# Kernel optimization log

Measured on AMD Instinct MI355X. Metric: run time of the kernel, lower is better.

Reference implementation:

```python
import jax, jax.numpy as jnp
import numpy as np

D_MODEL = 1024
NUM_HEADS = 16
HEAD_DIM = D_MODEL // NUM_HEADS
B, S = 2, 2048


def setup_inputs() -> dict:
    key = jax.random.key(0)
    ks = jax.random.split(key, 10)
    sc = 1.0 / np.sqrt(D_MODEL)
    return {
        "x": jax.random.normal(ks[0], (B, S, D_MODEL), jnp.float32),
        "y": jax.random.normal(ks[1], (B, S, D_MODEL), jnp.float32),
        "Wkv": jax.random.normal(ks[2], (D_MODEL, 2 * D_MODEL), jnp.float32) * sc,
        "bkv": jax.random.normal(ks[3], (2 * D_MODEL,), jnp.float32) * 0.01,
        "Wq": jax.random.normal(ks[4], (D_MODEL, D_MODEL), jnp.float32) * sc,
        "bq": jax.random.normal(ks[5], (D_MODEL,), jnp.float32) * 0.01,
        "Wo": jax.random.normal(ks[6], (D_MODEL, D_MODEL), jnp.float32) * sc,
        "bo": jax.random.normal(ks[7], (D_MODEL,), jnp.float32) * 0.01,
    }


def reference(x, y, Wkv, bkv, Wq, bq, Wo, bo):
    b, s, d = x.shape
    # projections: kv from x (keys/values come from encoder side), q from y
    kv = x @ Wkv + bkv                      # [B, S, 2*d_model]
    q = y @ Wq + bq                         # [B, S, d_model]
    kv = kv.reshape(b, s, NUM_HEADS, 2 * HEAD_DIM).transpose(0, 2, 1, 3)  # [B,H,S,2*hd]
    q = q.reshape(b, s, NUM_HEADS, HEAD_DIM).transpose(0, 2, 1, 3)        # [B,H,S,hd]
    k, v = jnp.split(kv, 2, axis=-1)        # each [B,H,S,hd]
    scaled = jnp.einsum("bhqd,bhkd->bhqk", q, k) / np.sqrt(HEAD_DIM)      # [B,H,S,S]
    attention = jax.nn.softmax(scaled, axis=-1)
    values = jnp.einsum("bhqk,bhkd->bhqd", attention, v)                  # [B,H,S,hd]
    values = values.transpose(0, 2, 1, 3).reshape(b, s, d)                # [B,S,d_model]
    return values @ Wo + bo
```

## Files before the change

### kernel.cpp

```cpp
#include <hip/hip_runtime.h>
#include <hip/hip_bf16.h>

typedef __attribute__((ext_vector_type(8))) short short8;
typedef __attribute__((ext_vector_type(4))) short short4v;
typedef __attribute__((ext_vector_type(4))) float f32x4;

#define B_  2
#define S_  2048
#define H_  16
#define HD_ 64
#define D_  1024
#define QSCALE 0.18033688f

__device__ __forceinline__ short f2bs(float f) {
  union { float f; unsigned u; } c; c.f = f;
  unsigned u = c.u;
  u += 0x7fffu + ((u >> 16) & 1u);
  return (short)(u >> 16);
}

__device__ __forceinline__ float bs2f(short v) {
  union { unsigned u; float f; } c;
  c.u = ((unsigned)(unsigned short)v) << 16;
  return c.f;
}

__device__ __forceinline__ unsigned pack_bf16(float a, float b) {
  __hip_bfloat162 h = __float22bfloat162_rn(float2{a, b});
  return *reinterpret_cast<unsigned*>(&h);
}

__device__ __forceinline__ float fexp2(float x) {
#if __has_builtin(__builtin_amdgcn_exp2f)
  return __builtin_amdgcn_exp2f(x);
#else
  return exp2f(x);
#endif
}

__device__ __forceinline__ float frcp(float x) {
#if __has_builtin(__builtin_amdgcn_rcpf)
  return __builtin_amdgcn_rcpf(x);
#else
  return 1.0f / x;
#endif
}

#define GL2LDS(gp, lp) __builtin_amdgcn_global_load_lds( \
    (const __attribute__((address_space(1))) unsigned int*)(gp), \
    (__attribute__((address_space(3))) unsigned int*)(lp), 16, 0, 0)

__global__ __launch_bounds__(256)
void prep_kernel(const float* __restrict__ x, const float* __restrict__ y,
                 short* __restrict__ xb, short* __restrict__ yb,
                 const float* __restrict__ Wkv, short* __restrict__ Wkvt,
                 const float* __restrict__ Wq, short* __restrict__ Wqt,
                 const float* __restrict__ Wo, short* __restrict__ Wot) {
  __shared__ float tile[64][65];
  int bx = blockIdx.x;
  if (bx < 8192) {
    int i = bx * 256 + threadIdx.x;
    const float4* src; short4v* dst; int j;
    if (i < (1 << 20)) { src = (const float4*)x; dst = (short4v*)xb; j = i; }
    else               { src = (const float4*)y; dst = (short4v*)yb; j = i - (1 << 20); }
    float4 f = src[j];
    short4v o;
    o.x = f2bs(f.x); o.y = f2bs(f.y); o.z = f2bs(f.z); o.w = f2bs(f.w);
    dst[j] = o;
    return;
  }
  bx -= 8192;
  const float* in; short* out; int C, c0, r0;
  if (bx < 512)      { in = Wkv; out = Wkvt; C = 2048; c0 = (bx & 31) * 64; r0 = (bx >> 5) * 64; }
  else if (bx < 768) { bx -= 512; in = Wq; out = Wqt; C = 1024; c0 = (bx & 15) * 64; r0 = (bx >> 4) * 64; }
  else               { bx -= 768; in = Wo; out = Wot; C = 1024; c0 = (bx & 15) * 64; r0 = (bx >> 4) * 64; }
  const int tx = threadIdx.x & 63, ty = threadIdx.x >> 6;
#pragma unroll
  for (int i = 0; i < 16; ++i) {
    int r = ty + i * 4;
    tile[r][tx] = in[(size_t)(r0 + r) * C + c0 + tx];
  }
  __syncthreads();
#pragma unroll
  for (int i = 0; i < 16; ++i) {
    int r = ty + i * 4;
    out[(size_t)(c0 + r) * 1024 + r0 + tx] = f2bs(tile[tx][r]);
  }
}

template <int MODE>
__device__ __forceinline__ void gemm_body8(const short* __restrict__ A, const short* __restrict__ Bt,
                                           const float* __restrict__ bias,
                                           void* __restrict__ out0, void* __restrict__ out1,
                                           int m0, int n0, int K, short* lds) {
  const int tid = threadIdx.x;
  const int w = tid >> 6, lane = tid & 63;
  const int q15 = lane & 15, quad = lane >> 4;
  const int xw = q15 & 7;
  const int wr = (w >> 1) * 32, wc = (w & 1) * 64;

  f32x4 acc[2][4];
#pragma unroll
  for (int i = 0; i < 2; ++i)
#pragma unroll
    for (int j = 0; j < 4; ++j) acc[i][j] = f32x4{0.f, 0.f, 0.f, 0.f};

  const int srow = w * 8 + (lane >> 3);
  const int gch  = (lane & 7) ^ (srow & 7);
  const int loff = w * 512 + lane * 8;
  const short* Ag = A + (size_t)(m0 + srow) * K + gch * 8;
  const short* Bg = Bt + (size_t)(n0 + srow) * K + gch * 8;

  GL2LDS(Ag,                  lds + loff);
  GL2LDS(Ag + (size_t)64 * K, lds + loff + 4096);
  GL2LDS(Bg,                  lds + 16384 + loff);
  GL2LDS(Bg + (size_t)64 * K, lds + 16384 + loff + 4096);

  const int NK = K >> 6;
  for (int kt = 0; kt < NK; ++kt) {
    __syncthreads();
    const short* Ac = lds + ((kt & 1) ? 8192 : 0);
    const short* Bc = lds + 16384 + ((kt & 1) ? 8192 : 0);
    if (kt < NK - 1) {
      const short* a2 = Ag + (kt + 1) * 64;
      const short* b2 = Bg + (kt + 1) * 64;
      short* ad = lds + ((kt & 1) ? 0 : 8192) + loff;
      short* bd = lds + 16384 + ((kt & 1) ? 0 : 8192) + loff;
      GL2LDS(a2,                  ad);
      GL2LDS(a2 + (size_t)64 * K, ad + 4096);
      GL2LDS(b2,                  bd);
      GL2LDS(b2 + (size_t)64 * K, bd + 4096);
    }
    short8 af[2][2], bf[4][2];
#pragma unroll
    for (int mi = 0; mi < 2; ++mi)
#pragma unroll
      for (int kk = 0; kk < 2; ++kk)
        af[mi][kk] = *(const short8*)(Ac + (wr + mi * 16 + q15) * 64 + (((kk * 4 + quad) ^ xw) * 8));
#pragma unroll
    for (int ni = 0; ni < 4; ++ni)
#pragma unroll
      for (int kk = 0; kk < 2; ++kk)
        bf[ni][kk] = *(const short8*)(Bc + (wc + ni * 16 + q15) * 64 + (((kk * 4 + quad) ^ xw) * 8));
#pragma unroll
    for (int mi = 0; mi < 2; ++mi)
#pragma unroll
      for (int ni = 0; ni < 4; ++ni)
#pragma unroll
        for (int kk = 0; kk < 2; ++kk)
          acc[mi][ni] = __builtin_amdgcn_mfma_f32_16x16x32_bf16(af[mi][kk], bf[ni][kk], acc[mi][ni], 0, 0, 0);
  }

  if constexpr (MODE == 0) {
#pragma unroll
    for (int mi = 0; mi < 2; ++mi)
#pragma unroll
      for (int ni = 0; ni < 4; ++ni) {
        const int n = n0 + wc + ni * 16 + q15;
        const float bn = bias[n];
#pragma unroll
        for (int r = 0; r < 4; ++r) {
          const int m = m0 + wr + mi * 16 + quad * 4 + r;
          int b = m >> 11, s = m & 2047, hh = n >> 6, d = n & 63;
          ((short*)out0)[((size_t)((b * H_ + hh) * S_ + s) << 6) + d] = f2bs((acc[mi][ni][r] + bn) * QSCALE);
        }
      }
  } else {
    const int hh = n0 >> 7;
    const int bb = m0 >> 11;
    const size_t bh = (size_t)(bb * H_ + hh);
    const int s0 = m0 & 2047;
    __syncthreads();
    short* VT = lds;
    if ((w & 1) == 0) {
#pragma unroll
      for (int mi = 0; mi < 2; ++mi)
#pragma unroll
        for (int ni = 0; ni < 4; ++ni) {
          const float bn = bias[n0 + ni * 16 + q15];
#pragma unroll
          for (int r = 0; r < 4; ++r) {
            const int s = s0 + wr + mi * 16 + quad * 4 + r;
            ((short*)out0)[((bh * S_ + s) << 6) + ni * 16 + q15] = f2bs(acc[mi][ni][r] + bn);
          }
        }
    } else {
#pragma unroll
      for (int mi = 0; mi < 2; ++mi)
#pragma unroll
        for (int ni = 0; ni < 4; ++ni) {
          const int d = ni * 16 + q15;
          const float bn = bias[n0 + 64 + d];
#pragma unroll
          for (int t = 0; t < 2; ++t) {
            const int chunk = (wr >> 1) + mi * 8 + quad * 2 + t;
            unsigned pk = pack_bf16(acc[mi][ni][2 * t] + bn, acc[mi][ni][2 * t + 1] + bn);
            *reinterpret_cast<unsigned*>(VT + d * 128 + ((chunk ^ (d & 15)) * 2)) = pk;
          }
        }
    }
    __syncthreads();
    {
      const int d = tid >> 3, t8 = tid & 7;
      unsigned vals[8];
#pragma unroll
      for (int c = 0; c < 8; ++c) {
        int chunk = t8 * 8 + c;
        vals[c] = *reinterpret_cast<unsigned*>(VT + d * 128 + ((chunk ^ (d & 15)) * 2));
      }
      uint4* dst = (uint4*)((short*)out1 + ((bh * HD_ + d) << 11) + s0 + t8 * 16);
      dst[0] = uint4{vals[0], vals[1], vals[2], vals[3]};
      dst[1] = uint4{vals[4], vals[5], vals[6], vals[7]};
    }
  }
}

__global__ __launch_bounds__(512, 4)
void proj_kernel(const short* __restrict__ xb, const short* __restrict__ Wkvt,
                 const float* __restrict__ bkv, short* __restrict__ Kb, short* __restrict__ Vtb,
                 const short* __restrict__ yb, const short* __restrict__ Wqt,
                 const float* __restrict__ bq, short* __restrict__ Qb) {
  __shared__ __align__(16) short lds[32768];
  int bx = blockIdx.x;
  if (bx < 512)
    gemm_body8<1>(xb, Wkvt, bkv, Kb, Vtb, (bx >> 4) * 128, (bx & 15) * 128, 1024, lds);
  else {
    bx -= 512;
    gemm_body8<0>(yb, Wqt, bq, Qb, nullptr, (bx >> 3) * 128, (bx & 7) * 128, 1024, lds);
  }
}

__global__ __launch_bounds__(256, 2)
void attn_kernel(const short* __restrict__ Q, const short* __restrict__ K,
                 const short* __restrict__ Vt, short* __restrict__ Obase,
                 float* __restrict__ Ls) {
  __shared__ __align__(16) short lds[32768];
  short* PQ = lds + 16384;
  const int tid = threadIdx.x;
  const int w = tid >> 6, lane = tid & 63;
  const int q15 = lane & 15, quad = lane >> 4;
  const int xw = q15 & 7;
  const int bx = blockIdx.x;
  const int xcd = bx & 7, slot = bx >> 3;
  const int pg = slot >> 4, rest = slot & 15;
  const int half = rest >> 3, qt = rest & 7;
  const int pp = xcd * 4 + pg;
  const int h = pp & 15, b = pp >> 4;
  const size_t bh = (size_t)(b * H_ + h);
  const short* Qg = Q + bh * (S_ * HD_) + qt * (256 * HD_);
  const short* Kg = K + bh * (S_ * HD_);
  const short* Vg = Vt + bh * (HD_ * S_);

  const int srow = w * 8 + (lane >> 3);
  const int gch  = (lane & 7) ^ (srow & 7);
  const int loff = w * 512 + lane * 8;

  {
    const short* qg = Qg + srow * 64 + gch * 8;
#pragma unroll
    for (int t = 0; t < 8; ++t) GL2LDS(qg + t * 2048, PQ + loff + t * 2048);
  }
  const short* kg = Kg + srow * 64 + gch * 8;
  const short* vg = Vg + (size_t)srow * S_ + gch * 8;
  const int kt0 = half * 16;
  GL2LDS(kg + kt0 * 4096,          lds + loff);
  GL2LDS(kg + kt0 * 4096 + 2048,   lds + loff + 2048);
  GL2LDS(vg + kt0 * 64,                    lds + 8192 + loff);
  GL2LDS(vg + kt0 * 64 + (size_t)32 * S_,  lds + 8192 + loff + 2048);
  __syncthreads();

  short8 aq[4][2];
#pragma unroll
  for (int st = 0; st < 4; ++st)
#pragma unroll
    for (int kk = 0; kk < 2; ++kk)
      aq[st][kk] = *(const short8*)(PQ + (w * 64 + st * 16 + q15) * 64 + (((kk * 4 + quad) ^ xw) * 8));
  short* Psw = PQ + w * 4096;

  f32x4 oacc[4][4];
#pragma unroll
  for (int st = 0; st < 4; ++st)
#pragma unroll
    for (int ni = 0; ni < 4; ++ni) oacc[st][ni] = f32x4{0.f, 0.f, 0.f, 0.f};
  float lsum[4] = {0.f, 0.f, 0.f, 0.f};
  const f32x4 zz = {0.f, 0.f, 0.f, 0.f};

  for (int kt = 0; kt < 16; ++kt) {
    __syncthreads();
    const short* Kc = lds + ((kt & 1) ? 4096 : 0);
    const short* Vc = lds + 8192 + ((kt & 1) ? 4096 : 0);
    if (kt < 15) {
      const int kn = kt0 + kt + 1;
      short* kd = lds + ((kt & 1) ? 0 : 4096) + loff;
      short* vd = lds + 8192 + ((kt & 1) ? 0 : 4096) + loff;
      GL2LDS(kg + kn * 4096,          kd);
      GL2LDS(kg + kn * 4096 + 2048,   kd + 2048);
      GL2LDS(vg + kn * 64,                    vd);
      GL2LDS(vg + kn * 64 + (size_t)32 * S_,  vd + 2048);
    }

    short8 ka[4][2];
#pragma unroll
    for (int mi = 0; mi < 4; ++mi) {
      const short* kr = Kc + (mi * 16 + q15) * 64;
      ka[mi][0] = *(const short8*)(kr + ((quad ^ xw) * 8));
      ka[mi][1] = *(const short8*)(kr + (((quad + 4) ^ xw) * 8));
    }

#pragma unroll
    for (int st = 0; st < 4; ++st) {
      short* Pst = Psw + st * 1024;
#pragma unroll
      for (int mi = 0; mi < 4; ++mi) {
        f32x4 t = __builtin_amdgcn_mfma_f32_16x16x32_bf16(ka[mi][0], aq[st][0], zz, 0, 0, 0);
        f32x4 s = __builtin_amdgcn_mfma_f32_16x16x32_bf16(ka[mi][1], aq[st][1], t, 0, 0, 0);
        float p0 = fexp2(s[0]), p1 = fexp2(s[1]), p2 = fexp2(s[2]), p3 = fexp2(s[3]);
        lsum[st] += (p0 + p1) + (p2 + p3);
        uint2 pk;
        pk.x = pack_bf16(p0, p1);
        pk.y = pack_bf16(p2, p3);
        *reinterpret_cast<uint2*>(Pst + q15 * 64 + (((mi * 2 + (quad >> 1)) ^ xw) * 8) + (quad & 1) * 4) = pk;
      }
    }

    short8 ap[4][2];
#pragma unroll
    for (int st = 0; st < 4; ++st)
#pragma unroll
      for (int kk = 0; kk < 2; ++kk)
        ap[st][kk] = *(const short8*)(Psw + st * 1024 + q15 * 64 + (((kk * 4 + quad) ^ xw) * 8));
#pragma unroll
    for (int ni = 0; ni < 4; ++ni) {
      const short* vr = Vc + (ni * 16 + q15) * 64;
#pragma unroll
      for (int kk = 0; kk < 2; ++kk) {
        short8 bv = *(const short8*)(vr + (((kk * 4 + quad) ^ xw) * 8));
#pragma unroll
        for (int st = 0; st < 4; ++st)
          oacc[st][ni] = __builtin_amdgcn_mfma_f32_16x16x32_bf16(ap[st][kk], bv, oacc[st][ni], 0, 0, 0);
      }
    }
  }

  short* Op = Obase + (size_t)half * (4 << 20);
#pragma unroll
  for (int st = 0; st < 4; ++st) {
    float l = lsum[st];
    l += __shfl_xor(l, 16);
    l += __shfl_xor(l, 32);
    const int qrow = qt * 256 + w * 64 + st * 16;
    if (quad == 0)
      Ls[half * 65536 + (int)bh * 2048 + qrow + q15] = l;
#pragma unroll
    for (int ni = 0; ni < 4; ++ni) {
      const int col = h * HD_ + ni * 16 + q15;
#pragma unroll
      for (int r = 0; r < 4; ++r) {
        const int m = b * S_ + qrow + quad * 4 + r;
        Op[(size_t)m * D_ + col] = f2bs(oacc[st][ni][r]);
      }
    }
  }
}

__global__ __launch_bounds__(512, 4)
void gemm_o_kernel(const short* __restrict__ O0, const short* __restrict__ O1,
                   const float* __restrict__ Ls,
                   const short* __restrict__ Bt, const float* __restrict__ bias,
                   float* __restrict__ out) {
  __shared__ __align__(16) short lds[32768];
  const int tid = threadIdx.x;
  const int w = tid >> 6, lane = tid & 63;
  const int q15 = lane & 15, quad = lane >> 4;
  const int xw = q15 & 7;
  const int m0 = blockIdx.y * 128, n0 = blockIdx.x * 128;
  const int wr = (w >> 1) * 32, wc = (w & 1) * 64;

  f32x4 acc[2][4];
#pragma unroll
  for (int i = 0; i < 2; ++i)
#pragma unroll
    for (int j = 0; j < 4; ++j) acc[i][j] = f32x4{0.f, 0.f, 0.f, 0.f};

  const int srow = w * 8 + (lane >> 3);
  const int gch  = (lane & 7) ^ (srow & 7);
  const int loff = w * 512 + lane * 8;
  const int bb = m0 >> 11;
  const int s1 = (m0 & 2047) + srow;
  const short* Bg = Bt + (size_t)(n0 + srow) * 1024 + gch * 8;

  GL2LDS(Bg,             lds + 16384 + loff);
  GL2LDS(Bg + 64 * 1024, lds + 16384 + loff + 4096);
  {
    const size_t ro = (size_t)(m0 + srow) * 1024 + gch * 8;
    short8 a0 = *(const short8*)(O0 + ro);
    short8 e0 = *(const short8*)(O1 + ro);
    short8 a1 = *(const short8*)(O0 + ro + 64 * 1024);
    short8 e1 = *(const short8*)(O1 + ro + 64 * 1024);
    const int li = bb * 16 * 2048;
    float inv0 = frcp(Ls[li + s1] + Ls[65536 + li + s1]);
    float inv1 = frcp(Ls[li + s1 + 64] + Ls[65536 + li + s1 + 64]);
    short8 v0, v1;
#pragma unroll
    for (int i = 0; i < 8; ++i) {
      v0[i] = f2bs((bs2f(a0[i]) + bs2f(e0[i])) * inv0);
      v1[i] = f2bs((bs2f(a1[i]) + bs2f(e1[i])) * inv1);
    }
    *(short8*)(lds + loff) = v0;
    *(short8*)(lds + loff + 4096) = v1;
  }

  for (int kt = 0; kt < 16; ++kt) {
    __syncthreads();
    const short* Ac = lds + ((kt & 1) ? 8192 : 0);
    const short* Bc = lds + 16384 + ((kt & 1) ? 8192 : 0);

    short8 a0, e0, a1, e1;
    float L00, L01, L10, L11;
    if (kt < 15) {
      const size_t ro = (size_t)(m0 + srow) * 1024 + (kt + 1) * 64 + gch * 8;
      a0 = *(const short8*)(O0 + ro);
      e0 = *(const short8*)(O1 + ro);
      a1 = *(const short8*)(O0 + ro + 64 * 1024);
      e1 = *(const short8*)(O1 + ro + 64 * 1024);
      const int li = (bb * 16 + kt + 1) * 2048;
      L00 = Ls[li + s1];      L01 = Ls[65536 + li + s1];
      L10 = Ls[li + s1 + 64]; L11 = Ls[65536 + li + s1 + 64];
      const short* b2 = Bg + (kt + 1) * 64;
      short* bd = lds + 16384 + ((kt & 1) ? 0 : 8192) + loff;
      GL2LDS(b2,             bd);
      GL2LDS(b2 + 64 * 1024, bd + 4096);
    }

    short8 af[2][2], bf[4][2];
#pragma unroll
    for (int mi = 0; mi < 2; ++mi)
#pragma unroll
      for (int kk = 0; kk < 2; ++kk)
        af[mi][kk] = *(const short8*)(Ac + (wr + mi * 16 + q15) * 64 + (((kk * 4 + quad) ^ xw) * 8));
#pragma unroll
    for (int ni = 0; ni < 4; ++ni)
#pragma unroll
      for (int kk = 0; kk < 2; ++kk)
        bf[ni][kk] = *(const short8*)(Bc + (wc + ni * 16 + q15) * 64 + (((kk * 4 + quad) ^ xw) * 8));
#pragma unroll
    for (int mi = 0; mi < 2; ++mi)
#pragma unroll
      for (int ni = 0; ni < 4; ++ni)
#pragma unroll
        for (int kk = 0; kk < 2; ++kk)
          acc[mi][ni] = __builtin_amdgcn_mfma_f32_16x16x32_bf16(af[mi][kk], bf[ni][kk], acc[mi][ni], 0, 0, 0);

    if (kt < 15) {
      float inv0 = frcp(L00 + L01);
      float inv1 = frcp(L10 + L11);
      short8 v0, v1;
#pragma unroll
      for (int i = 0; i < 8; ++i) {
        v0[i] = f2bs((bs2f(a0[i]) + bs2f(e0[i])) * inv0);
        v1[i] = f2bs((bs2f(a1[i]) + bs2f(e1[i])) * inv1);
      }
      short* ad = lds + ((kt & 1) ? 0 : 8192) + loff;
      *(short8*)(ad) = v0;
      *(short8*)(ad + 4096) = v1;
    }
  }

#pragma unroll
  for (int mi = 0; mi < 2; ++mi)
#pragma unroll
    for (int ni = 0; ni < 4; ++ni) {
      const int n = n0 + wc + ni * 16 + q15;
      const float bn = bias[n];
#pragma unroll
      for (int r = 0; r < 4; ++r) {
        const int m = m0 + wr + mi * 16 + quad * 4 + r;
        out[(size_t)m * 1024 + n] = acc[mi][ni][r] + bn;
      }
    }
}

extern "C" void kernel_launch(void* const* d_in, const int* in_sizes, int n_in,
                              void* d_out, int out_size, void* d_ws, size_t ws_size,
                              hipStream_t stream) {
  const float* x   = (const float*)d_in[0];
  const float* y   = (const float*)d_in[1];
  const float* Wkv = (const float*)d_in[2];
  const float* bkv = (const float*)d_in[3];
  const float* Wq  = (const float*)d_in[4];
  const float* bq  = (const float*)d_in[5];
  const float* Wo  = (const float*)d_in[6];
  const float* bo  = (const float*)d_in[7];
  float* out = (float*)d_out;

  short* xb   = (short*)d_ws;
  short* yb   = xb + (4 << 20);
  short* Wkvt = yb + (4 << 20);
  short* Wqt  = Wkvt + (2 << 20);
  short* Wot  = Wqt + (1 << 20);
  short* Kb   = Wot + (1 << 20);
  short* Vtb  = Kb + (4 << 20);
  short* Qb   = Vtb + (4 << 20);
  short* LsR  = Qb + (4 << 20);
  float* Ls   = (float*)LsR;

  prep_kernel<<<9216, 256, 0, stream>>>(x, y, xb, yb, Wkv, Wkvt, Wq, Wqt, Wo, Wot);
  proj_kernel<<<768, 512, 0, stream>>>(xb, Wkvt, bkv, Kb, Vtb, yb, Wqt, bq, Qb);
  attn_kernel<<<512, 256, 0, stream>>>(Qb, Kb, Vtb, xb, Ls);
  gemm_o_kernel<<<dim3(8, 32), 512, 0, stream>>>(xb, yb, Ls, Wot, bo, out);
}
```

Baseline: 213.4 us.

## Halve attention and output-GEMM tile heights to double grid size and occupancy

The attention kernel now processes 128 query rows per block instead of 256. That doubles the grid to 1024 blocks, cuts LDS use, and raises the occupancy target to 3 blocks per SIMD. The P·V step is now interleaved per query subtile with V fragments held in registers, shrinking the per-wave P scratch. The output GEMM uses 64-row M tiles with a new A-loading map, doubling its grid to 512 blocks. This spreads work over more CUs at the cost of less reuse of K/V and Wo tiles per block and more redundant global loads.

```diff
diff --git a/kernel.cpp b/kernel.cpp
--- a/kernel.cpp
+++ b/kernel.cpp
@@ -230,24 +230,23 @@
   }
 }
 
-__global__ __launch_bounds__(256, 2)
+__global__ __launch_bounds__(256, 3)
 void attn_kernel(const short* __restrict__ Q, const short* __restrict__ K,
-                 const short* __restrict__ Vt, short* __restrict__ Obase,
-                 float* __restrict__ Ls) {
-  __shared__ __align__(16) short lds[32768];
-  short* PQ = lds + 16384;
+                 const short* __restrict__ Vt, short* __restrict__ O0,
+                 short* __restrict__ O1, float* __restrict__ Ls) {
+  __shared__ __align__(16) short lds[20480];
   const int tid = threadIdx.x;
   const int w = tid >> 6, lane = tid & 63;
   const int q15 = lane & 15, quad = lane >> 4;
   const int xw = q15 & 7;
   const int bx = blockIdx.x;
   const int xcd = bx & 7, slot = bx >> 3;
-  const int pg = slot >> 4, rest = slot & 15;
-  const int half = rest >> 3, qt = rest & 7;
+  const int pg = slot >> 5, rest = slot & 31;
+  const int half = rest >> 4, qt = rest & 15;
   const int pp = xcd * 4 + pg;
   const int h = pp & 15, b = pp >> 4;
   const size_t bh = (size_t)(b * H_ + h);
-  const short* Qg = Q + bh * (S_ * HD_) + qt * (256 * HD_);
+  const short* Qg = Q + bh * (S_ * HD_) + qt * (128 * HD_);
   const short* Kg = K + bh * (S_ * HD_);
   const short* Vg = Vt + bh * (HD_ * S_);
 
@@ -258,8 +257,17 @@
   {
     const short* qg = Qg + srow * 64 + gch * 8;
 #pragma unroll
-    for (int t = 0; t < 8; ++t) GL2LDS(qg + t * 2048, PQ + loff + t * 2048);
-  }
+    for (int t = 0; t < 4; ++t) GL2LDS(qg + t * 2048, lds + loff + t * 2048);
+  }
+  __syncthreads();
+  short8 aq[2][2];
+#pragma unroll
+  for (int st = 0; st < 2; ++st)
+#pragma unroll
+    for (int kk = 0; kk < 2; ++kk)
+      aq[st][kk] = *(const short8*)(lds + (w * 32 + st * 16 + q15) * 64 + (((kk * 4 + quad) ^ xw) * 8));
+  __syncthreads();
+
   const short* kg = Kg + srow * 64 + gch * 8;
   const short* vg = Vg + (size_t)srow * S_ + gch * 8;
   const int kt0 = half * 16;
@@ -267,22 +275,15 @@
   GL2LDS(kg + kt0 * 4096 + 2048,   lds + loff + 2048);
   GL2LDS(vg + kt0 * 64,                    lds + 8192 + loff);
   GL2LDS(vg + kt0 * 64 + (size_t)32 * S_,  lds + 8192 + loff + 2048);
-  __syncthreads();
-
-  short8 aq[4][2];
-#pragma unroll
-  for (int st = 0; st < 4; ++st)
-#pragma unroll
-    for (int kk = 0; kk < 2; ++kk)
-      aq[st][kk] = *(const short8*)(PQ + (w * 64 + st * 16 + q15) * 64 + (((kk * 4 + quad) ^ xw) * 8));
-  short* Psw = PQ + w * 4096;
-
-  f32x4 oacc[4][4];
-#pragma unroll
-  for (int st = 0; st < 4; ++st)
+
+  short* Pw = lds + 16384 + w * 1024;
+
+  f32x4 oacc[2][4];
+#pragma unroll
+  for (int st = 0; st < 2; ++st)
 #pragma unroll
     for (int ni = 0; ni < 4; ++ni) oacc[st][ni] = f32x4{0.f, 0.f, 0.f, 0.f};
-  float lsum[4] = {0.f, 0.f, 0.f, 0.f};
+  float lsum[2] = {0.f, 0.f};
   const f32x4 zz = {0.f, 0.f, 0.f, 0.f};
 
   for (int kt = 0; kt < 16; ++kt) {
@@ -299,17 +300,19 @@
       GL2LDS(vg + kn * 64 + (size_t)32 * S_,  vd + 2048);
     }
 
-    short8 ka[4][2];
+    short8 ka[4][2], bv[4][2];
 #pragma unroll
     for (int mi = 0; mi < 4; ++mi) {
       const short* kr = Kc + (mi * 16 + q15) * 64;
       ka[mi][0] = *(const short8*)(kr + ((quad ^ xw) * 8));
       ka[mi][1] = *(const short8*)(kr + (((quad + 4) ^ xw) * 8));
-    }
-
-#pragma unroll
-    for (int st = 0; st < 4; ++st) {
-      short* Pst = Psw + st * 1024;
+      const short* vr = Vc + (mi * 16 + q15) * 64;
+      bv[mi][0] = *(const short8*)(vr + ((quad ^ xw) * 8));
+      bv[mi][1] = *(const short8*)(vr + (((quad + 4) ^ xw) * 8));
+    }
+
+#pragma unroll
+    for (int st = 0; st < 2; ++st) {
 #pragma unroll
       for (int mi = 0; mi < 4; ++mi) {
         f32x4 t = __builtin_amdgcn_mfma_f32_16x16x32_bf16(ka[mi][0], aq[st][0], zz, 0, 0, 0);
@@ -319,36 +322,27 @@
         uint2 pk;
         pk.x = pack_bf16(p0, p1);
         pk.y = pack_bf16(p2, p3);
-        *reinterpret_cast<uint2*>(Pst + q15 * 64 + (((mi * 2 + (quad >> 1)) ^ xw) * 8) + (quad & 1) * 4) = pk;
+        *reinterpret_cast<uint2*>(Pw + q15 * 64 + (((mi * 2 + (quad >> 1)) ^ xw) * 8) + (quad & 1) * 4) = pk;
       }
-    }
-
-    short8 ap[4][2];
-#pragma unroll
-    for (int st = 0; st < 4; ++st)
+      short8 ap[2];
 #pragma unroll
       for (int kk = 0; kk < 2; ++kk)
-        ap[st][kk] = *(const short8*)(Psw + st * 1024 + q15 * 64 + (((kk * 4 + quad) ^ xw) * 8));
-#pragma unroll
-    for (int ni = 0; ni < 4; ++ni) {
-      const short* vr = Vc + (ni * 16 + q15) * 64;
-#pragma unroll
-      for (int kk = 0; kk < 2; ++kk) {
-        short8 bv = *(const short8*)(vr + (((kk * 4 + quad) ^ xw) * 8));
-#pragma unroll
-        for (int st = 0; st < 4; ++st)
-          oacc[st][ni] = __builtin_amdgcn_mfma_f32_16x16x32_bf16(ap[st][kk], bv, oacc[st][ni], 0, 0, 0);
-      }
-    }
-  }
-
-  short* Op = Obase + (size_t)half * (4 << 20);
-#pragma unroll
-  for (int st = 0; st < 4; ++st) {
+        ap[kk] = *(const short8*)(Pw + q15 * 64 + (((kk * 4 + quad) ^ xw) * 8));
+#pragma unroll
+      for (int ni = 0; ni < 4; ++ni)
+#pragma unroll
+        for (int kk = 0; kk < 2; ++kk)
+          oacc[st][ni] = __builtin_amdgcn_mfma_f32_16x16x32_bf16(ap[kk], bv[ni][kk], oacc[st][ni], 0, 0, 0);
+    }
+  }
+
+  short* Op = half ? O1 : O0;
+#pragma unroll
+  for (int st = 0; st < 2; ++st) {
     float l = lsum[st];
     l += __shfl_xor(l, 16);
     l += __shfl_xor(l, 32);
-    const int qrow = qt * 256 + w * 64 + st * 16;
+    const int qrow = qt * 128 + w * 32 + st * 16;
     if (quad == 0)
       Ls[half * 65536 + (int)bh * 2048 + qrow + q15] = l;
 #pragma unroll
@@ -368,116 +362,94 @@
                    const float* __restrict__ Ls,
                    const short* __restrict__ Bt, const float* __restrict__ bias,
                    float* __restrict__ out) {
-  __shared__ __align__(16) short lds[32768];
+  __shared__ __align__(16) short lds[24576];
   const int tid = threadIdx.x;
   const int w = tid >> 6, lane = tid & 63;
   const int q15 = lane & 15, quad = lane >> 4;
   const int xw = q15 & 7;
-  const int m0 = blockIdx.y * 128, n0 = blockIdx.x * 128;
-  const int wr = (w >> 1) * 32, wc = (w & 1) * 64;
-
-  f32x4 acc[2][4];
-#pragma unroll
-  for (int i = 0; i < 2; ++i)
-#pragma unroll
-    for (int j = 0; j < 4; ++j) acc[i][j] = f32x4{0.f, 0.f, 0.f, 0.f};
-
+  const int m0 = blockIdx.y * 64, n0 = blockIdx.x * 128;
+  const int wr = (w >> 1) * 16, wc = (w & 1) * 64;
+
+  f32x4 acc[4];
+#pragma unroll
+  for (int j = 0; j < 4; ++j) acc[j] = f32x4{0.f, 0.f, 0.f, 0.f};
+
+  const int rowA = tid >> 3, s8 = tid & 7;
+  const int gchA = s8 ^ (rowA & 7);
+  const int bb = m0 >> 11;
+  const int s1 = (m0 & 2047) + rowA;
   const int srow = w * 8 + (lane >> 3);
-  const int gch  = (lane & 7) ^ (srow & 7);
+  const int gchB = (lane & 7) ^ (srow & 7);
   const int loff = w * 512 + lane * 8;
-  const int bb = m0 >> 11;
-  const int s1 = (m0 & 2047) + srow;
-  const short* Bg = Bt + (size_t)(n0 + srow) * 1024 + gch * 8;
-
-  GL2LDS(Bg,             lds + 16384 + loff);
-  GL2LDS(Bg + 64 * 1024, lds + 16384 + loff + 4096);
+  const short* Bg = Bt + (size_t)(n0 + srow) * 1024 + gchB * 8;
+
+  GL2LDS(Bg,             lds + 8192 + loff);
+  GL2LDS(Bg + 64 * 1024, lds + 8192 + loff + 4096);
   {
-    const size_t ro = (size_t)(m0 + srow) * 1024 + gch * 8;
+    const size_t ro = (size_t)(m0 + rowA) * 1024 + gchA * 8;
     short8 a0 = *(const short8*)(O0 + ro);
     short8 e0 = *(const short8*)(O1 + ro);
-    short8 a1 = *(const short8*)(O0 + ro + 64 * 1024);
-    short8 e1 = *(const short8*)(O1 + ro + 64 * 1024);
-    const int li = bb * 16 * 2048;
-    float inv0 = frcp(Ls[li + s1] + Ls[65536 + li + s1]);
-    float inv1 = frcp(Ls[li + s1 + 64] + Ls[65536 + li + s1 + 64]);
-    short8 v0, v1;
-#pragma unroll
-    for (int i = 0; i < 8; ++i) {
-      v0[i] = f2bs((bs2f(a0[i]) + bs2f(e0[i])) * inv0);
-      v1[i] = f2bs((bs2f(a1[i]) + bs2f(e1[i])) * inv1);
-    }
-    *(short8*)(lds + loff) = v0;
-    *(short8*)(lds + loff + 4096) = v1;
+    const int li = bb * 16 * 2048 + s1;
+    float inv = frcp(Ls[li] + Ls[65536 + li]);
+    short8 v;
+#pragma unroll
+    for (int i = 0; i < 8; ++i) v[i] = f2bs((bs2f(a0[i]) + bs2f(e0[i])) * inv);
+    *(short8*)(lds + rowA * 64 + s8 * 8) = v;
   }
 
   for (int kt = 0; kt < 16; ++kt) {
     __syncthreads();
-    const short* Ac = lds + ((kt & 1) ? 8192 : 0);
-    const short* Bc = lds + 16384 + ((kt & 1) ? 8192 : 0);
-
-    short8 a0, e0, a1, e1;
-    float L00, L01, L10, L11;
+    const short* Ac = lds + ((kt & 1) ? 4096 : 0);
+    const short* Bc = lds + 8192 + ((kt & 1) ? 8192 : 0);
+
+    short8 a0, e0;
+    float L0, L1;
     if (kt < 15) {
-      const size_t ro = (size_t)(m0 + srow) * 1024 + (kt + 1) * 64 + gch * 8;
+      const size_t ro = (size_t)(m0 + rowA) * 1024 + (kt + 1) * 64 + gchA * 8;
       a0 = *(const short8*)(O0 + ro);
       e0 = *(const short8*)(O1 + ro);
-      a1 = *(const short8*)(O0 + ro + 64 * 1024);
-      e1 = *(const short8*)(O1 + ro + 64 * 1024);
-      const int li = (bb * 16 + kt + 1) * 2048;
-      L00 = Ls[li + s1];      L01 = Ls[65536 + li + s1];
-      L10 = Ls[li + s1 + 64]; L11 = Ls[65536 + li + s1 + 64];
+      const int li = (bb * 16 + kt + 1) * 2048 + s1;
+      L0 = Ls[li]; L1 = Ls[65536 + li];
       const short* b2 = Bg + (kt + 1) * 64;
-      short* bd = lds + 16384 + ((kt & 1) ? 0 : 8192) + loff;
+      short* bd = lds + 8192 + ((kt & 1) ? 0 : 8192) + loff;
       GL2LDS(b2,             bd);
       GL2LDS(b2 + 64 * 1024, bd + 4096);
     }
 
-    short8 af[2][2], bf[4][2];
-#pragma unroll
-    for (int mi = 0; mi < 2; ++mi)
-#pragma unroll
-      for (int kk = 0; kk < 2; ++kk)
-        af[mi][kk] = *(const short8*)(Ac + (wr + mi * 16 + q15) * 64 + (((kk * 4 + quad) ^ xw) * 8));
+    short8 af[2], bf[4][2];
+#pragma unroll
+    for (int kk = 0; kk < 2; ++kk)
+      af[kk] = *(const short8*)(Ac + (wr + q15) * 64 + (((kk * 4 + quad) ^ xw) * 8));
 #pragma unroll
     for (int ni = 0; ni < 4; ++ni)
 #pragma unroll
       for (int kk = 0; kk < 2; ++kk)
         bf[ni][kk] = *(const short8*)(Bc + (wc + ni * 16 + q15) * 64 + (((kk * 4 + quad) ^ xw) * 8));
 #pragma unroll
-    for (int mi = 0; mi < 2; ++mi)
-#pragma unroll
-      for (int ni = 0; ni < 4; ++ni)
-#pragma unroll
-        for (int kk = 0; kk < 2; ++kk)
-          acc[mi][ni] = __builtin_amdgcn_mfma_f32_16x16x32_bf16(af[mi][kk], bf[ni][kk], acc[mi][ni], 0, 0, 0);
+    for (int ni = 0; ni < 4; ++ni)
+#pragma unroll
+      for (int kk = 0; kk < 2; ++kk)
+        acc[ni] = __builtin_amdgcn_mfma_f32_16x16x32_bf16(af[kk], bf[ni][kk], acc[ni], 0, 0, 0);
 
     if (kt < 15) {
-      float inv0 = frcp(L00 + L01);
-      float inv1 = frcp(L10 + L11);
-      short8 v0, v1;
-#pragma unroll
-      for (int i = 0; i < 8; ++i) {
-        v0[i] = f2bs((bs2f(a0[i]) + bs2f(e0[i])) * inv0);
-        v1[i] = f2bs((bs2f(a1[i]) + bs2f(e1[i])) * inv1);
-      }
-      short* ad = lds + ((kt & 1) ? 0 : 8192) + loff;
-      *(short8*)(ad) = v0;
-      *(short8*)(ad + 4096) = v1;
-    }
-  }
-
-#pragma unroll
-  for (int mi = 0; mi < 2; ++mi)
-#pragma unroll
-    for (int ni = 0; ni < 4; ++ni) {
-      const int n = n0 + wc + ni * 16 + q15;
-      const float bn = bias[n];
-#pragma unroll
-      for (int r = 0; r < 4; ++r) {
-        const int m = m0 + wr + mi * 16 + quad * 4 + r;
-        out[(size_t)m * 1024 + n] = acc[mi][ni][r] + bn;
-      }
-    }
+      float inv = frcp(L0 + L1);
+      short8 v;
+#pragma unroll
+      for (int i = 0; i < 8; ++i) v[i] = f2bs((bs2f(a0[i]) + bs2f(e0[i])) * inv);
+      *(short8*)(lds + ((kt & 1) ? 0 : 4096) + rowA * 64 + s8 * 8) = v;
+    }
+  }
+
+#pragma unroll
+  for (int ni = 0; ni < 4; ++ni) {
+    const int n = n0 + wc + ni * 16 + q15;
+    const float bn = bias[n];
+#pragma unroll
+    for (int r = 0; r < 4; ++r) {
+      const int m = m0 + wr + quad * 4 + r;
+      out[(size_t)m * 1024 + n] = acc[ni][r] + bn;
+    }
+  }
 }
 
 extern "C" void kernel_launch(void* const* d_in, const int* in_sizes, int n_in,
@@ -506,6 +478,6 @@
 
   prep_kernel<<<9216, 256, 0, stream>>>(x, y, xb, yb, Wkv, Wkvt, Wq, Wqt, Wo, Wot);
   proj_kernel<<<768, 512, 0, stream>>>(xb, Wkvt, bkv, Kb, Vtb, yb, Wqt, bq, Qb);
-  attn_kernel<<<512, 256, 0, stream>>>(Qb, Kb, Vtb, xb, Ls);
-  gemm_o_kernel<<<dim3(8, 32), 512, 0, stream>>>(xb, yb, Ls, Wot, bo, out);
-}
+  attn_kernel<<<1024, 256, 0, stream>>>(Qb, Kb, Vtb, xb, yb, Ls);
+  gemm_o_kernel<<<dim3(8, 64), 512, 0, stream>>>(xb, yb, Ls, Wot, bo, out);
+}
```

Result: no change. 212.0 us (-0.6%).
